# Optimization experiments

Hardware: AMD Instinct MI355X
Metric: run time of the kernel (lower is better)

Reference implementation:

```python
import jax, jax.numpy as jnp
import numpy as np

DIM = 1024
HEADS = 16
HEAD_DIM = DIM // HEADS


def setup_inputs() -> dict:
    key = jax.random.key(0)
    k1, k2, k3 = jax.random.split(key, 3)
    x = jax.random.normal(k1, (4, 4096, DIM), dtype=jnp.float32)
    # nn.Linear weights; stored as [out, in] in torch, apply as x @ W.T
    w_qkv = jax.random.normal(k2, (3 * DIM, DIM), dtype=jnp.float32) * (1.0 / np.sqrt(DIM))
    w_out = jax.random.normal(k3, (DIM, DIM), dtype=jnp.float32) * (1.0 / np.sqrt(DIM))
    return {"x": x, "w_qkv": w_qkv, "w_out": w_out}


def _feature_map(t):
    # ELU + 1 (always positive)
    return jax.nn.elu(t) + 1.0


def reference(x, w_qkv, w_out):
    b, n, _ = x.shape
    qkv = x @ w_qkv.T  # [b, n, 3*dim]
    q, k, v = jnp.split(qkv, 3, axis=-1)
    # [b, n, dim] -> [b, h, n, d]
    def to_heads(t):
        return t.reshape(b, n, HEADS, HEAD_DIM).transpose(0, 2, 1, 3)
    q, k, v = to_heads(q), to_heads(k), to_heads(v)
    q = _feature_map(q)
    k = _feature_map(k)
    # KV state: [b, h, d, e]
    kv = jnp.einsum('bhnd,bhne->bhde', k, v)
    out = jnp.einsum('bhnd,bhde->bhne', q, kv)  # [b, h, n, e]
    k_sum = k.sum(axis=2)  # [b, h, d]
    normalizer = jnp.einsum('bhnd,bhd->bhn', q, k_sum)  # [b, h, n]
    out = out / (normalizer[..., None] + 1e-06)
    out = out.transpose(0, 2, 1, 3).reshape(b, n, DIM)
    return out @ w_out.T
```

## Files before the change

kernel.cpp:

```cpp
#include <hip/hip_runtime.h>
#include <hip/hip_bf16.h>
#include <stdint.h>

typedef __attribute__((ext_vector_type(8))) short short8;
typedef __attribute__((ext_vector_type(4))) float f32x4;
typedef __attribute__((ext_vector_type(4))) unsigned short ushort4_t;

#define SEG 16

__device__ __forceinline__ float bf2f(unsigned short u) {
  unsigned int x = ((unsigned int)u) << 16;
  return __uint_as_float(x);
}
__device__ __forceinline__ unsigned short f2bf(float f) {
  unsigned int u = __float_as_uint(f);
  u += 0x7fffu + ((u >> 16) & 1u);
  return (unsigned short)(u >> 16);
}

__device__ __forceinline__ void gload16(const unsigned short* g, unsigned short* l) {
  __builtin_amdgcn_global_load_lds(
      (const __attribute__((address_space(1))) void*)g,
      (__attribute__((address_space(3))) void*)l, 16, 0, 0);
}

__global__ void cast_f32_bf16(const float* __restrict__ in,
                              unsigned short* __restrict__ out, int n4) {
  const int stride = gridDim.x * blockDim.x;
  for (int i = blockIdx.x * blockDim.x + threadIdx.x; i < n4; i += stride) {
    const float4 v = ((const float4*)in)[i];
    ushort4_t o;
    o[0] = f2bf(v.x); o[1] = f2bf(v.y); o[2] = f2bf(v.z); o[3] = f2bf(v.w);
    ((ushort4_t*)out)[i] = o;
  }
}

template <typename OutT>
__global__ __launch_bounds__(512, 2) void gemm256(
    const unsigned short* __restrict__ A, const unsigned short* __restrict__ Bm,
    OutT* __restrict__ C, int M, int N, int K, int ldc, int fm_cols) {
  __shared__ unsigned short lds[4 * 16384];
  const int tid = threadIdx.x;
  const int lane = tid & 63;
  const int w = tid >> 6;
  const int wr = w >> 2, wc = w & 3;
  const int gx = gridDim.x;
  const int nwg = gx * gridDim.y;
  const int hwid = blockIdx.y * gx + blockIdx.x;
  const int cpx = nwg >> 3;
  const int L = (hwid & 7) * cpx + (hwid >> 3);
  const int bx = L % gx, by = L / gx;
  const size_t arow0 = (size_t)by * 256;
  const size_t bcol0 = (size_t)bx * 256;
  const int nt = K >> 5;

  const int rseg = lane >> 2;
  const int sc = (((lane & 3) ^ (rseg & 3)) << 3);
  const unsigned short* Aseg0 = A + (arow0 + w * 16 + rseg) * K + sc;
  const unsigned short* Aseg1 = A + (arow0 + (w + 8) * 16 + rseg) * K + sc;
  const unsigned short* Bseg0 = Bm + (bcol0 + w * 16 + rseg) * K + sc;
  const unsigned short* Bseg1 = Bm + (bcol0 + (w + 8) * 16 + rseg) * K + sc;

  auto stage = [&](int kt, int slot) {
    const int k0 = kt << 5;
    unsigned short* buf = lds + slot * 16384;
    gload16(Aseg0 + k0, buf + w * 512);
    gload16(Aseg1 + k0, buf + (w + 8) * 512);
    gload16(Bseg0 + k0, buf + 8192 + w * 512);
    gload16(Bseg1 + k0, buf + 8192 + (w + 8) * 512);
  };

  f32x4 acc[8][4] = {};
  const int fr = lane & 15;
  const int kc = lane >> 4;

  stage(0, 0);
  stage(1, 1);
  stage(2, 2);
  asm volatile("s_waitcnt vmcnt(8)" ::: "memory");
  __builtin_amdgcn_s_barrier();
  __builtin_amdgcn_sched_barrier(0);

  for (int t = 0; t < nt; ++t) {
    const int nx = (t + 3 < nt) ? t + 3 : t + 3 - nt;
    stage(nx, (t + 3) & 3);
    const unsigned short* buf = lds + (t & 3) * 16384;
    short8 af[8], bfv[4];
#pragma unroll
    for (int m = 0; m < 8; ++m) {
      const int r = wr * 128 + m * 16 + fr;
      af[m] = *(const short8*)&buf[r * 32 + ((kc ^ (r & 3)) << 3)];
    }
#pragma unroll
    for (int n = 0; n < 4; ++n) {
      const int r = wc * 64 + n * 16 + fr;
      bfv[n] = *(const short8*)&buf[8192 + r * 32 + ((kc ^ (r & 3)) << 3)];
    }
    __builtin_amdgcn_s_setprio(1);
#pragma unroll
    for (int m = 0; m < 8; ++m)
#pragma unroll
      for (int n = 0; n < 4; ++n)
        acc[m][n] = __builtin_amdgcn_mfma_f32_16x16x32_bf16(af[m], bfv[n], acc[m][n], 0, 0, 0);
    __builtin_amdgcn_s_setprio(0);
    asm volatile("s_waitcnt vmcnt(8)" ::: "memory");
    __builtin_amdgcn_s_barrier();
    __builtin_amdgcn_sched_barrier(0);
  }

  const int qq = lane >> 4;
#pragma unroll
  for (int m = 0; m < 8; ++m) {
#pragma unroll
    for (int n = 0; n < 4; ++n) {
      const int col = (int)bcol0 + wc * 64 + n * 16 + fr;
      const bool dofm = col < fm_cols;
#pragma unroll
      for (int j = 0; j < 4; ++j) {
        const int row = (int)arow0 + wr * 128 + m * 16 + qq * 4 + j;
        float x = acc[m][n][j];
        if (dofm) x = (x > 0.f) ? x + 1.f : __expf(x);
        if constexpr (sizeof(OutT) == 2) {
          C[(size_t)row * ldc + col] = (OutT)f2bf(x);
        } else {
          C[(size_t)row * ldc + col] = x;
        }
      }
    }
  }
}

__global__ __launch_bounds__(256) void kv_partial(
    const unsigned short* __restrict__ kvmat, float* __restrict__ kvp,
    float* __restrict__ ksp) {
  const int blk = blockIdx.x;
  const int bh = blk >> 4;
  const int seg = blk & (SEG - 1);
  const int b = bh >> 4, h = bh & 15;
  const int rows = 4096 / SEG;
  const size_t row0 = (size_t)b * 4096 + (size_t)seg * rows;
  const unsigned short* kb = kvmat + row0 * 2048 + h * 64;
  const unsigned short* vb = kvmat + row0 * 2048 + 1024 + h * 64;
  __shared__ float kl[32][64];
  __shared__ float vl[32][64];
  const int tid = threadIdx.x;
  const int d0 = (tid >> 4) * 4, e0 = (tid & 15) * 4;
  const int lr = tid >> 3, lc = (tid & 7) * 8;
  float accm[4][4] = {};
  float ksacc[4] = {0.f, 0.f, 0.f, 0.f};

  for (int c = 0; c < rows; c += 32) {
    __syncthreads();
    {
      const short8 k8 = *(const short8*)(kb + (size_t)(c + lr) * 2048 + lc);
      const short8 v8 = *(const short8*)(vb + (size_t)(c + lr) * 2048 + lc);
#pragma unroll
      for (int j = 0; j < 8; ++j) {
        kl[lr][lc + j] = bf2f((unsigned short)k8[j]);
        vl[lr][lc + j] = bf2f((unsigned short)v8[j]);
      }
    }
    __syncthreads();
#pragma unroll
    for (int r = 0; r < 32; ++r) {
      const f32x4 kd = *(const f32x4*)&kl[r][d0];
      const f32x4 ve = *(const f32x4*)&vl[r][e0];
#pragma unroll
      for (int i = 0; i < 4; ++i) {
        ksacc[i] += kd[i];
#pragma unroll
        for (int j = 0; j < 4; ++j) accm[i][j] += kd[i] * ve[j];
      }
    }
  }
  float* kvout = kvp + ((size_t)seg * 64 + bh) * 4096;
#pragma unroll
  for (int i = 0; i < 4; ++i) {
    f32x4 o = {accm[i][0], accm[i][1], accm[i][2], accm[i][3]};
    *(f32x4*)&kvout[(d0 + i) * 64 + e0] = o;
  }
  if ((tid & 15) == 0) {
#pragma unroll
    for (int i = 0; i < 4; ++i)
      ksp[((size_t)seg * 64 + bh) * 64 + d0 + i] = ksacc[i];
  }
}

__global__ void kv_reduce_bf(const float* __restrict__ kvp, const float* __restrict__ ksp,
                             unsigned short* __restrict__ kvb) {
  const int idx = blockIdx.x * 256 + threadIdx.x;
  if (idx >= 64 * 80 * 64) return;
  const int bh = idx / 5120, r = idx % 5120, e = r >> 6, d = r & 63;
  float s = 0.f;
  if (e < 64) {
    for (int g = 0; g < SEG; ++g) s += kvp[((size_t)g * 64 + bh) * 4096 + d * 64 + e];
  } else if (e == 64) {
    for (int g = 0; g < SEG; ++g) s += ksp[((size_t)g * 64 + bh) * 64 + d];
  }
  kvb[idx] = f2bf(s);
}

__global__ __launch_bounds__(256) void attn_mfma(
    const unsigned short* __restrict__ q,
    const unsigned short* __restrict__ kvb,
    unsigned short* __restrict__ att) {
  const int bh = blockIdx.x >> 4;
  const int rt = blockIdx.x & 15;
  const int b = bh >> 4, h = bh & 15;
  __shared__ unsigned short As[2 * 256 * 32];
  __shared__ unsigned short Bs[2 * 80 * 32];
  const int tid = threadIdx.x, lane = tid & 63, wave = tid >> 6;
  const int l4 = lane >> 2;
  const int c8 = (lane & 3) * 8;
  const size_t qrow0 = (size_t)b * 4096 + (size_t)rt * 256;
  const unsigned short* Ab = q + (qrow0 + wave * 64 + l4) * 1024 + h * 64 + c8;
  unsigned short* AsW = As;
#pragma unroll
  for (int ks = 0; ks < 2; ++ks)
#pragma unroll
    for (int i = 0; i < 4; ++i)
      gload16(Ab + (size_t)i * 16 * 1024 + ks * 32,
              AsW + ks * 8192 + wave * 2048 + i * 512);
  for (int c = tid; c < 640; c += 256) {
    const int m0 = c * 8, ks = m0 / 2560, rr = m0 % 2560, e = rr / 32, dk = rr % 32;
    *(short8*)&Bs[m0] = *(const short8*)&kvb[(size_t)bh * 5120 + e * 64 + ks * 32 + dk];
  }
  __syncthreads();

  const int fr = lane & 15, ko = (lane >> 4) * 8;
  short8 af[4][2], bfv[5][2];
#pragma unroll
  for (int m = 0; m < 4; ++m)
#pragma unroll
    for (int ks = 0; ks < 2; ++ks)
      af[m][ks] = *(const short8*)&As[ks * 8192 + (wave * 64 + m * 16 + fr) * 32 + ko];
#pragma unroll
  for (int n = 0; n < 5; ++n)
#pragma unroll
    for (int ks = 0; ks < 2; ++ks)
      bfv[n][ks] = *(const short8*)&Bs[ks * 2560 + (n * 16 + fr) * 32 + ko];
  f32x4 acc[4][5] = {};
#pragma unroll
  for (int m = 0; m < 4; ++m)
#pragma unroll
    for (int n = 0; n < 5; ++n) {
      acc[m][n] = __builtin_amdgcn_mfma_f32_16x16x32_bf16(af[m][0], bfv[n][0], acc[m][n], 0, 0, 0);
      acc[m][n] = __builtin_amdgcn_mfma_f32_16x16x32_bf16(af[m][1], bfv[n][1], acc[m][n], 0, 0, 0);
    }

  const int qq = lane >> 4;
#pragma unroll
  for (int m = 0; m < 4; ++m) {
    f32x4 rnv;
#pragma unroll
    for (int j = 0; j < 4; ++j) {
      const float nv = __shfl(acc[m][4][j], lane & 48);
      rnv[j] = 1.f / (nv + 1e-6f);
    }
    const size_t row = qrow0 + wave * 64 + m * 16 + qq * 4;
#pragma unroll
    for (int n = 0; n < 4; ++n)
#pragma unroll
      for (int j = 0; j < 4; ++j)
        att[(row + j) * 1024 + h * 64 + n * 16 + fr] = f2bf(acc[m][n][j] * rnv[j]);
  }
}

extern "C" void kernel_launch(void* const* d_in, const int* in_sizes, int n_in,
                              void* d_out, int out_size, void* d_ws, size_t ws_size,
                              hipStream_t stream) {
  const float* x = (const float*)d_in[0];
  const float* wqkv = (const float*)d_in[1];
  const float* wout = (const float*)d_in[2];
  float* out = (float*)d_out;

  char* ws = (char*)d_ws;
  size_t off = 0;
  auto alloc = [&](size_t bytes) -> void* {
    void* p = ws + off;
    off += (bytes + 255) & ~(size_t)255;
    return p;
  };
  unsigned short* xbf    = (unsigned short*)alloc((size_t)16384 * 1024 * 2);
  unsigned short* wqkvbf = (unsigned short*)alloc((size_t)3072 * 1024 * 2);
  unsigned short* woutbf = (unsigned short*)alloc((size_t)1024 * 1024 * 2);
  unsigned short* big    = (unsigned short*)alloc((size_t)16384 * 2048 * 2);
  float* kvp = (float*)alloc((size_t)SEG * 64 * 4096 * 4);
  float* ksp = (float*)alloc((size_t)SEG * 64 * 64 * 4);
  unsigned short* kvb = (unsigned short*)alloc((size_t)64 * 80 * 64 * 2);
  unsigned short* qbuf = big;
  unsigned short* att  = big + (size_t)16384 * 1024;

  cast_f32_bf16<<<2048, 256, 0, stream>>>(x, xbf, 16384 * 1024 / 4);
  cast_f32_bf16<<<1024, 256, 0, stream>>>(wqkv, wqkvbf, 3072 * 1024 / 4);
  cast_f32_bf16<<<512, 256, 0, stream>>>(wout, woutbf, 1024 * 1024 / 4);

  gemm256<unsigned short><<<dim3(2048 / 256, 16384 / 256), 512, 0, stream>>>(
      xbf, wqkvbf + (size_t)1024 * 1024, big, 16384, 2048, 1024, 2048, 1024);

  kv_partial<<<64 * SEG, 256, 0, stream>>>(big, kvp, ksp);
  kv_reduce_bf<<<1280, 256, 0, stream>>>(kvp, ksp, kvb);

  gemm256<unsigned short><<<dim3(1024 / 256, 16384 / 256), 512, 0, stream>>>(
      xbf, wqkvbf, qbuf, 16384, 1024, 1024, 1024, 1024);

  attn_mfma<<<64 * 16, 256, 0, stream>>>(qbuf, kvb, att);

  gemm256<float><<<dim3(1024 / 256, 16384 / 256), 512, 0, stream>>>(
      att, woutbf, out, 16384, 1024, 1024, 1024, 0);
}
```

Baseline: 268.1 us.

## Restructure GEMM into eight-phase ping-pong pipeline with 64-wide K tiles

Replaces the 4-slot, K=32 GEMM main loop with a double-buffered A/B scheme using K=64 tiles and an 8-phase schedule. Each phase interleaves LDS fragment reads, global-to-LDS prefetch of one half-tile and a quarter of the MFMA block, with barriers between phases. The LDS swizzle changes to an 8-way XOR for the wider rows. The aim is finer overlap of memory loads with MFMA work and fewer per-iteration barriers per K element, at the cost of more barriers overall and more complex wait-count bookkeeping.

New measurement: 258.1 us. 1.04x faster.

```diff
diff --git a/kernel.cpp b/kernel.cpp
--- a/kernel.cpp
+++ b/kernel.cpp
@@ -35,11 +35,20 @@
   }
 }
 
+#define MIDBAR() do { __builtin_amdgcn_sched_barrier(0); __builtin_amdgcn_s_barrier(); } while (0)
+#define ENDBAR() do { __builtin_amdgcn_s_barrier(); __builtin_amdgcn_sched_barrier(0); } while (0)
+#define ENDBARV() do { asm volatile("s_waitcnt vmcnt(4)" ::: "memory"); \
+                       __builtin_amdgcn_s_barrier(); __builtin_amdgcn_sched_barrier(0); } while (0)
+
 template <typename OutT>
-__global__ __launch_bounds__(512, 2) void gemm256(
+__global__ __launch_bounds__(512, 2) void gemm8p(
     const unsigned short* __restrict__ A, const unsigned short* __restrict__ Bm,
     OutT* __restrict__ C, int M, int N, int K, int ldc, int fm_cols) {
-  __shared__ unsigned short lds[4 * 16384];
+  __shared__ unsigned short lds[65536];
+  unsigned short* A0 = lds;
+  unsigned short* B0 = lds + 16384;
+  unsigned short* A1 = lds + 32768;
+  unsigned short* B1 = lds + 49152;
   const int tid = threadIdx.x;
   const int lane = tid & 63;
   const int w = tid >> 6;
@@ -52,60 +61,96 @@
   const int bx = L % gx, by = L / gx;
   const size_t arow0 = (size_t)by * 256;
   const size_t bcol0 = (size_t)bx * 256;
-  const int nt = K >> 5;
-
-  const int rseg = lane >> 2;
-  const int sc = (((lane & 3) ^ (rseg & 3)) << 3);
-  const unsigned short* Aseg0 = A + (arow0 + w * 16 + rseg) * K + sc;
-  const unsigned short* Aseg1 = A + (arow0 + (w + 8) * 16 + rseg) * K + sc;
-  const unsigned short* Bseg0 = Bm + (bcol0 + w * 16 + rseg) * K + sc;
-  const unsigned short* Bseg1 = Bm + (bcol0 + (w + 8) * 16 + rseg) * K + sc;
-
-  auto stage = [&](int kt, int slot) {
-    const int k0 = kt << 5;
-    unsigned short* buf = lds + slot * 16384;
-    gload16(Aseg0 + k0, buf + w * 512);
-    gload16(Aseg1 + k0, buf + (w + 8) * 512);
-    gload16(Bseg0 + k0, buf + 8192 + w * 512);
-    gload16(Bseg1 + k0, buf + 8192 + (w + 8) * 512);
-  };
-
+  const int nt = K >> 6;
+  const int nit = nt >> 1;
+
+  const int sc8 = ((lane & 7) ^ (lane >> 3)) << 3;
+  const unsigned short* Abase = A + (arow0 + (lane >> 3)) * K + sc8;
+  const unsigned short* Bbase = Bm + (bcol0 + (lane >> 3)) * K + sc8;
+
+  auto stage = [&](int kt, const unsigned short* mb, unsigned short* region, int half) {
+    const int ktw = (kt >= nt) ? kt - nt : kt;
+    const int rb = half * 128 + w * 16;
+    const unsigned short* s = mb + (size_t)rb * K + ktw * 64;
+    gload16(s, region + rb * 64);
+    gload16(s + (size_t)8 * K, region + (rb + 8) * 64);
+  };
+
+  short8 af[4][2];
+  short8 bfv[4][2];
   f32x4 acc[8][4] = {};
   const int fr = lane & 15;
   const int kc = lane >> 4;
 
-  stage(0, 0);
-  stage(1, 1);
-  stage(2, 2);
-  asm volatile("s_waitcnt vmcnt(8)" ::: "memory");
+  auto readA = [&](const unsigned short* bufA, int mh) {
+#pragma unroll
+    for (int mm = 0; mm < 4; ++mm) {
+      const int r = wr * 128 + (mh * 4 + mm) * 16 + fr;
+#pragma unroll
+      for (int ks = 0; ks < 2; ++ks)
+        af[mm][ks] = *(const short8*)&bufA[r * 64 + (((ks * 4 + kc) ^ (fr & 7)) << 3)];
+    }
+  };
+  auto readB = [&](const unsigned short* bufB, int nh) {
+#pragma unroll
+    for (int nn = 0; nn < 2; ++nn) {
+      const int n = nh * 2 + nn;
+      const int r = wc * 64 + n * 16 + fr;
+#pragma unroll
+      for (int ks = 0; ks < 2; ++ks)
+        bfv[n][ks] = *(const short8*)&bufB[16384 * 0 + r * 64 + (((ks * 4 + kc) ^ (fr & 7)) << 3)];
+    }
+  };
+  auto quad = [&](int mh, int nh) {
+    __builtin_amdgcn_s_setprio(1);
+#pragma unroll
+    for (int mm = 0; mm < 4; ++mm)
+#pragma unroll
+      for (int nn = 0; nn < 2; ++nn) {
+        f32x4& a = acc[mh * 4 + mm][nh * 2 + nn];
+        a = __builtin_amdgcn_mfma_f32_16x16x32_bf16(af[mm][0], bfv[nh * 2 + nn][0], a, 0, 0, 0);
+        a = __builtin_amdgcn_mfma_f32_16x16x32_bf16(af[mm][1], bfv[nh * 2 + nn][1], a, 0, 0, 0);
+      }
+    __builtin_amdgcn_s_setprio(0);
+  };
+
+  stage(0, Abase, A0, 0); stage(0, Abase, A0, 1);
+  stage(0, Bbase, B0, 0); stage(0, Bbase, B0, 1);
+  stage(1, Bbase, B1, 0); stage(1, Bbase, B1, 1);
+  asm volatile("s_waitcnt vmcnt(0)" ::: "memory");
   __builtin_amdgcn_s_barrier();
   __builtin_amdgcn_sched_barrier(0);
 
-  for (int t = 0; t < nt; ++t) {
-    const int nx = (t + 3 < nt) ? t + 3 : t + 3 - nt;
-    stage(nx, (t + 3) & 3);
-    const unsigned short* buf = lds + (t & 3) * 16384;
-    short8 af[8], bfv[4];
-#pragma unroll
-    for (int m = 0; m < 8; ++m) {
-      const int r = wr * 128 + m * 16 + fr;
-      af[m] = *(const short8*)&buf[r * 32 + ((kc ^ (r & 3)) << 3)];
-    }
-#pragma unroll
-    for (int n = 0; n < 4; ++n) {
-      const int r = wc * 64 + n * 16 + fr;
-      bfv[n] = *(const short8*)&buf[8192 + r * 32 + ((kc ^ (r & 3)) << 3)];
-    }
-    __builtin_amdgcn_s_setprio(1);
-#pragma unroll
-    for (int m = 0; m < 8; ++m)
-#pragma unroll
-      for (int n = 0; n < 4; ++n)
-        acc[m][n] = __builtin_amdgcn_mfma_f32_16x16x32_bf16(af[m], bfv[n], acc[m][n], 0, 0, 0);
-    __builtin_amdgcn_s_setprio(0);
-    asm volatile("s_waitcnt vmcnt(8)" ::: "memory");
-    __builtin_amdgcn_s_barrier();
-    __builtin_amdgcn_sched_barrier(0);
+  for (int i2 = 0; i2 < nit; ++i2) {
+    const int t0 = i2 * 2;
+    readA(A0, 0); readB(B0, 0);
+    stage(t0 + 1, Abase, A1, 0);
+    MIDBAR(); quad(0, 0); ENDBAR();
+
+    readB(B0, 1);
+    stage(t0 + 1, Abase, A1, 1);
+    MIDBAR(); quad(0, 1); ENDBAR();
+
+    readA(A0, 1);
+    stage(t0 + 2, Bbase, B0, 0);
+    MIDBAR(); quad(1, 0); ENDBAR();
+
+    stage(t0 + 2, Bbase, B0, 1);
+    MIDBAR(); quad(1, 1); ENDBARV();
+    readA(A1, 0); readB(B1, 0);
+    stage(t0 + 2, Abase, A0, 0);
+    MIDBAR(); quad(0, 0); ENDBAR();
+
+    readB(B1, 1);
+    stage(t0 + 2, Abase, A0, 1);
+    MIDBAR(); quad(0, 1); ENDBAR();
+
+    readA(A1, 1);
+    stage(t0 + 3, Bbase, B1, 0);
+    MIDBAR(); quad(1, 0); ENDBAR();
+
+    stage(t0 + 3, Bbase, B1, 1);
+    MIDBAR(); quad(1, 1); ENDBARV();
   }
 
   const int qq = lane >> 4;
@@ -295,17 +340,17 @@
   cast_f32_bf16<<<1024, 256, 0, stream>>>(wqkv, wqkvbf, 3072 * 1024 / 4);
   cast_f32_bf16<<<512, 256, 0, stream>>>(wout, woutbf, 1024 * 1024 / 4);
 
-  gemm256<unsigned short><<<dim3(2048 / 256, 16384 / 256), 512, 0, stream>>>(
+  gemm8p<unsigned short><<<dim3(2048 / 256, 16384 / 256), 512, 0, stream>>>(
       xbf, wqkvbf + (size_t)1024 * 1024, big, 16384, 2048, 1024, 2048, 1024);
 
   kv_partial<<<64 * SEG, 256, 0, stream>>>(big, kvp, ksp);
   kv_reduce_bf<<<1280, 256, 0, stream>>>(kvp, ksp, kvb);
 
-  gemm256<unsigned short><<<dim3(1024 / 256, 16384 / 256), 512, 0, stream>>>(
+  gemm8p<unsigned short><<<dim3(1024 / 256, 16384 / 256), 512, 0, stream>>>(
       xbf, wqkvbf, qbuf, 16384, 1024, 1024, 1024, 1024);
 
   attn_mfma<<<64 * 16, 256, 0, stream>>>(qbuf, kvb, att);
 
-  gemm256<float><<<dim3(1024 / 256, 16384 / 256), 512, 0, stream>>>(
+  gemm8p<float><<<dim3(1024 / 256, 16384 / 256), 512, 0, stream>>>(
       att, woutbf, out, 16384, 1024, 1024, 1024, 0);
 }
```

## Replace GEMM with 256x128 tile, double-buffered, interleaved load/MFMA phases

Applied to the files above, without the earlier changes.

Rewrites the GEMM kernel to use 256x128 output tiles with 8 waves arranged 4x2, each computing 64x64. A double-buffered LDS scheme replaces the previous 4-deep one, and the per-iteration global loads are split into three chunks interleaved with four MFMA phases separated by barriers. Occupancy is raised via launch_bounds(512,4) with smaller LDS. The aim is more concurrent workgroups and finer load/compute overlap, at the cost of more barriers per k-step, a full vmcnt(0) wait each iteration, and lower per-tile arithmetic intensity.

After: 266.5 us. About the same (-0.6%).

```diff
diff --git a/kernel.cpp b/kernel.cpp
--- a/kernel.cpp
+++ b/kernel.cpp
@@ -35,15 +35,18 @@
   }
 }
 
+#define MIDBAR() do { __builtin_amdgcn_sched_barrier(0); __builtin_amdgcn_s_barrier(); } while (0)
+#define ENDBAR() do { __builtin_amdgcn_s_barrier(); __builtin_amdgcn_sched_barrier(0); } while (0)
+
 template <typename OutT>
-__global__ __launch_bounds__(512, 2) void gemm256(
+__global__ __launch_bounds__(512, 4) void gemm_v3(
     const unsigned short* __restrict__ A, const unsigned short* __restrict__ Bm,
     OutT* __restrict__ C, int M, int N, int K, int ldc, int fm_cols) {
-  __shared__ unsigned short lds[4 * 16384];
+  __shared__ unsigned short lds[2 * 12288];
   const int tid = threadIdx.x;
   const int lane = tid & 63;
   const int w = tid >> 6;
-  const int wr = w >> 2, wc = w & 3;
+  const int wr = w >> 1, wc = w & 1;
   const int gx = gridDim.x;
   const int nwg = gx * gridDim.y;
   const int hwid = blockIdx.y * gx + blockIdx.x;
@@ -51,73 +54,99 @@
   const int L = (hwid & 7) * cpx + (hwid >> 3);
   const int bx = L % gx, by = L / gx;
   const size_t arow0 = (size_t)by * 256;
-  const size_t bcol0 = (size_t)bx * 256;
+  const size_t bcol0 = (size_t)bx * 128;
   const int nt = K >> 5;
 
-  const int rseg = lane >> 2;
-  const int sc = (((lane & 3) ^ (rseg & 3)) << 3);
-  const unsigned short* Aseg0 = A + (arow0 + w * 16 + rseg) * K + sc;
-  const unsigned short* Aseg1 = A + (arow0 + (w + 8) * 16 + rseg) * K + sc;
-  const unsigned short* Bseg0 = Bm + (bcol0 + w * 16 + rseg) * K + sc;
-  const unsigned short* Bseg1 = Bm + (bcol0 + (w + 8) * 16 + rseg) * K + sc;
-
-  auto stage = [&](int kt, int slot) {
-    const int k0 = kt << 5;
-    unsigned short* buf = lds + slot * 16384;
-    gload16(Aseg0 + k0, buf + w * 512);
-    gload16(Aseg1 + k0, buf + (w + 8) * 512);
-    gload16(Bseg0 + k0, buf + 8192 + w * 512);
-    gload16(Bseg1 + k0, buf + 8192 + (w + 8) * 512);
-  };
-
-  f32x4 acc[8][4] = {};
+  const int rl = lane >> 2;
+  const int sce = (((lane & 3) ^ (rl & 3)) << 3);
+  const unsigned short* Ab0 = A + (arow0 + w * 16 + rl) * K + sce;
+  const unsigned short* Ab1 = A + (arow0 + 128 + w * 16 + rl) * K + sce;
+  const unsigned short* Bb0 = Bm + (bcol0 + w * 16 + rl) * K + sce;
+
+  auto stageA0 = [&](int kt, unsigned short* buf) {
+    gload16(Ab0 + ((kt < nt ? kt : kt - nt) << 5), buf + w * 512);
+  };
+  auto stageA1 = [&](int kt, unsigned short* buf) {
+    gload16(Ab1 + ((kt < nt ? kt : kt - nt) << 5), buf + 4096 + w * 512);
+  };
+  auto stageB = [&](int kt, unsigned short* buf) {
+    gload16(Bb0 + ((kt < nt ? kt : kt - nt) << 5), buf + 8192 + w * 512);
+  };
+
+  f32x4 acc[4][4] = {};
   const int fr = lane & 15;
   const int kc = lane >> 4;
 
-  stage(0, 0);
-  stage(1, 1);
-  stage(2, 2);
-  asm volatile("s_waitcnt vmcnt(8)" ::: "memory");
+  auto rdA = [&](const unsigned short* buf, int mm) {
+    const int r = wr * 64 + mm * 16 + fr;
+    return *(const short8*)&buf[r * 32 + ((kc ^ (r & 3)) << 3)];
+  };
+  auto rdB = [&](const unsigned short* buf, int nn) {
+    const int r = wc * 64 + nn * 16 + fr;
+    return *(const short8*)&buf[8192 + r * 32 + ((kc ^ (r & 3)) << 3)];
+  };
+
+  stageA0(0, lds); stageA1(0, lds); stageB(0, lds);
+  asm volatile("s_waitcnt vmcnt(0)" ::: "memory");
   __builtin_amdgcn_s_barrier();
   __builtin_amdgcn_sched_barrier(0);
 
   for (int t = 0; t < nt; ++t) {
-    const int nx = (t + 3 < nt) ? t + 3 : t + 3 - nt;
-    stage(nx, (t + 3) & 3);
-    const unsigned short* buf = lds + (t & 3) * 16384;
-    short8 af[8], bfv[4];
-#pragma unroll
-    for (int m = 0; m < 8; ++m) {
-      const int r = wr * 128 + m * 16 + fr;
-      af[m] = *(const short8*)&buf[r * 32 + ((kc ^ (r & 3)) << 3)];
-    }
-#pragma unroll
-    for (int n = 0; n < 4; ++n) {
-      const int r = wc * 64 + n * 16 + fr;
-      bfv[n] = *(const short8*)&buf[8192 + r * 32 + ((kc ^ (r & 3)) << 3)];
-    }
+    unsigned short* cur = lds + (t & 1) * 12288;
+    unsigned short* nxt = lds + ((t & 1) ^ 1) * 12288;
+    short8 af0, af1, af2, af3, bf0, bf1, bf2, bf3;
+    af0 = rdA(cur, 0); af1 = rdA(cur, 1);
+    bf0 = rdB(cur, 0); bf1 = rdB(cur, 1);
+    stageA0(t + 1, nxt);
+    MIDBAR();
     __builtin_amdgcn_s_setprio(1);
-#pragma unroll
-    for (int m = 0; m < 8; ++m)
-#pragma unroll
-      for (int n = 0; n < 4; ++n)
-        acc[m][n] = __builtin_amdgcn_mfma_f32_16x16x32_bf16(af[m], bfv[n], acc[m][n], 0, 0, 0);
+    acc[0][0] = __builtin_amdgcn_mfma_f32_16x16x32_bf16(af0, bf0, acc[0][0], 0, 0, 0);
+    acc[0][1] = __builtin_amdgcn_mfma_f32_16x16x32_bf16(af0, bf1, acc[0][1], 0, 0, 0);
+    acc[1][0] = __builtin_amdgcn_mfma_f32_16x16x32_bf16(af1, bf0, acc[1][0], 0, 0, 0);
+    acc[1][1] = __builtin_amdgcn_mfma_f32_16x16x32_bf16(af1, bf1, acc[1][1], 0, 0, 0);
     __builtin_amdgcn_s_setprio(0);
-    asm volatile("s_waitcnt vmcnt(8)" ::: "memory");
+    ENDBAR();
+    bf2 = rdB(cur, 2); bf3 = rdB(cur, 3);
+    stageA1(t + 1, nxt);
+    MIDBAR();
+    __builtin_amdgcn_s_setprio(1);
+    acc[0][2] = __builtin_amdgcn_mfma_f32_16x16x32_bf16(af0, bf2, acc[0][2], 0, 0, 0);
+    acc[0][3] = __builtin_amdgcn_mfma_f32_16x16x32_bf16(af0, bf3, acc[0][3], 0, 0, 0);
+    acc[1][2] = __builtin_amdgcn_mfma_f32_16x16x32_bf16(af1, bf2, acc[1][2], 0, 0, 0);
+    acc[1][3] = __builtin_amdgcn_mfma_f32_16x16x32_bf16(af1, bf3, acc[1][3], 0, 0, 0);
+    __builtin_amdgcn_s_setprio(0);
+    ENDBAR();
+    af2 = rdA(cur, 2); af3 = rdA(cur, 3);
+    stageB(t + 1, nxt);
+    MIDBAR();
+    __builtin_amdgcn_s_setprio(1);
+    acc[2][0] = __builtin_amdgcn_mfma_f32_16x16x32_bf16(af2, bf0, acc[2][0], 0, 0, 0);
+    acc[2][1] = __builtin_amdgcn_mfma_f32_16x16x32_bf16(af2, bf1, acc[2][1], 0, 0, 0);
+    acc[3][0] = __builtin_amdgcn_mfma_f32_16x16x32_bf16(af3, bf0, acc[3][0], 0, 0, 0);
+    acc[3][1] = __builtin_amdgcn_mfma_f32_16x16x32_bf16(af3, bf1, acc[3][1], 0, 0, 0);
+    __builtin_amdgcn_s_setprio(0);
+    ENDBAR();
+    __builtin_amdgcn_s_setprio(1);
+    acc[2][2] = __builtin_amdgcn_mfma_f32_16x16x32_bf16(af2, bf2, acc[2][2], 0, 0, 0);
+    acc[2][3] = __builtin_amdgcn_mfma_f32_16x16x32_bf16(af2, bf3, acc[2][3], 0, 0, 0);
+    acc[3][2] = __builtin_amdgcn_mfma_f32_16x16x32_bf16(af3, bf2, acc[3][2], 0, 0, 0);
+    acc[3][3] = __builtin_amdgcn_mfma_f32_16x16x32_bf16(af3, bf3, acc[3][3], 0, 0, 0);
+    __builtin_amdgcn_s_setprio(0);
+    asm volatile("s_waitcnt vmcnt(0)" ::: "memory");
     __builtin_amdgcn_s_barrier();
     __builtin_amdgcn_sched_barrier(0);
   }
 
   const int qq = lane >> 4;
 #pragma unroll
-  for (int m = 0; m < 8; ++m) {
+  for (int m = 0; m < 4; ++m) {
 #pragma unroll
     for (int n = 0; n < 4; ++n) {
       const int col = (int)bcol0 + wc * 64 + n * 16 + fr;
       const bool dofm = col < fm_cols;
 #pragma unroll
       for (int j = 0; j < 4; ++j) {
-        const int row = (int)arow0 + wr * 128 + m * 16 + qq * 4 + j;
+        const int row = (int)arow0 + wr * 64 + m * 16 + qq * 4 + j;
         float x = acc[m][n][j];
         if (dofm) x = (x > 0.f) ? x + 1.f : __expf(x);
         if constexpr (sizeof(OutT) == 2) {
@@ -295,17 +324,17 @@
   cast_f32_bf16<<<1024, 256, 0, stream>>>(wqkv, wqkvbf, 3072 * 1024 / 4);
   cast_f32_bf16<<<512, 256, 0, stream>>>(wout, woutbf, 1024 * 1024 / 4);
 
-  gemm256<unsigned short><<<dim3(2048 / 256, 16384 / 256), 512, 0, stream>>>(
+  gemm_v3<unsigned short><<<dim3(2048 / 128, 16384 / 256), 512, 0, stream>>>(
       xbf, wqkvbf + (size_t)1024 * 1024, big, 16384, 2048, 1024, 2048, 1024);
 
   kv_partial<<<64 * SEG, 256, 0, stream>>>(big, kvp, ksp);
   kv_reduce_bf<<<1280, 256, 0, stream>>>(kvp, ksp, kvb);
 
-  gemm256<unsigned short><<<dim3(1024 / 256, 16384 / 256), 512, 0, stream>>>(
+  gemm_v3<unsigned short><<<dim3(1024 / 128, 16384 / 256), 512, 0, stream>>>(
       xbf, wqkvbf, qbuf, 16384, 1024, 1024, 1024, 1024);
 
   attn_mfma<<<64 * 16, 256, 0, stream>>>(qbuf, kvb, att);
 
-  gemm256<float><<<dim3(1024 / 256, 16384 / 256), 512, 0, stream>>>(
+  gemm_v3<float><<<dim3(1024 / 128, 16384 / 256), 512, 0, stream>>>(
       att, woutbf, out, 16384, 1024, 1024, 1024, 0);
 }
```
